# Performance work log

Measured on AMD Instinct MI355X. Metric: run time of the kernel, lower is better.

Reference implementation:

```python
import jax, jax.numpy as jnp
import numpy as np

EPS_RMS = 1e-6
EPS_Q = 1e-5
EPS_NORM = 1e-10


def _rmsnorm(x):
    return x * jax.lax.rsqrt(jnp.mean(x * x, axis=-1, keepdims=True) + EPS_RMS)


def _activation_quant(x):
    # per-token 8-bit absmax quantization (BitNet b1.58)
    scale = 127.0 / jnp.maximum(jnp.max(jnp.abs(x), axis=-1, keepdims=True), EPS_Q)
    return jnp.clip(jnp.round(x * scale), -128.0, 127.0) / scale


def _weight_quant(w):
    # per-tensor ternary quantization with mean-abs scale
    scale = 1.0 / jnp.maximum(jnp.mean(jnp.abs(w)), EPS_Q)
    return jnp.clip(jnp.round(w * scale), -1.0, 1.0) / scale


def _bitlinear(x, w, b):
    xn = _rmsnorm(x)
    xq = xn + jax.lax.stop_gradient(_activation_quant(xn) - xn)  # STE
    wq = w + jax.lax.stop_gradient(_weight_quant(w) - w)         # STE
    return jnp.einsum('bsf,of->bso', xq, wq) + b


def setup_inputs() -> dict:
    key = jax.random.key(0)
    ks = jax.random.split(key, 4)
    B, S, F = 32, 1024, 512
    evidence_features = jax.random.normal(ks[0], (B, S, F), dtype=jnp.float32)
    prior_belief = jax.random.uniform(ks[1], (B, S, F), dtype=jnp.float32)
    W1 = jax.random.normal(ks[2], (F, 2 * F), dtype=jnp.float32) * (1.0 / np.sqrt(2 * F))
    b1 = jnp.zeros((F,), dtype=jnp.float32)
    W2 = jax.random.normal(ks[3], (F, F), dtype=jnp.float32) * (1.0 / np.sqrt(F))
    b2 = jnp.zeros((F,), dtype=jnp.float32)
    return {"evidence_features": evidence_features, "prior_belief": prior_belief,
            "W1": W1, "b1": b1, "W2": W2, "b2": b2}


def reference(evidence_features, prior_belief, W1, b1, W2, b2):
    # belief_update MLP on concat(prior, evidence)
    update_input = jnp.concatenate([prior_belief, evidence_features], axis=-1)  # [B,S,2F]
    h = jax.nn.relu(_bitlinear(update_input, W1, b1))                           # [B,S,F]
    likelihood_factors = jax.nn.sigmoid(_bitlinear(h, W2, b2))                  # [B,S,F]
    posterior_unnorm = prior_belief * likelihood_factors
    normalizer = jnp.maximum(jnp.sum(posterior_unnorm, axis=1, keepdims=True), EPS_NORM)
    return posterior_unnorm / normalizer
```

## Files before the change

kernel.cpp:

```cpp
#include <hip/hip_runtime.h>
#include <math.h>

typedef __attribute__((ext_vector_type(4))) int i32x4;
typedef __attribute__((ext_vector_type(4))) float f32x4;

#define GLOAD_LDS16(g, l)                                          \
  __builtin_amdgcn_global_load_lds(                                \
      (const __attribute__((address_space(1))) void*)(g),          \
      (__attribute__((address_space(3))) void*)(l), 16, 0, 0)

__global__ void kWabs(const float* __restrict__ w1, const float* __restrict__ w2,
                      double* __restrict__ part) {
  const bool second = blockIdx.x >= 256;
  const float* w = second ? w2 : w1;
  const int n = second ? 262144 : 524288;
  int t = (blockIdx.x & 255) * 256 + threadIdx.x;
  double s = 0.0;
  for (int i = t; i < n; i += 65536) s += (double)fabsf(w[i]);
#pragma unroll
  for (int m = 32; m >= 1; m >>= 1) s += __shfl_xor(s, m);
  __shared__ double sd[4];
  int lane = threadIdx.x & 63, wid = threadIdx.x >> 6;
  if (lane == 0) sd[wid] = s;
  __syncthreads();
  if (threadIdx.x == 0) part[blockIdx.x] = (sd[0] + sd[1]) + (sd[2] + sd[3]);
}

__global__ void kWfin(const double* __restrict__ part, float* __restrict__ wsv) {
  const double* p = part + blockIdx.x * 256;
  const double n = (blockIdx.x == 0) ? 524288.0 : 262144.0;
  double s = p[threadIdx.x];
#pragma unroll
  for (int m = 32; m >= 1; m >>= 1) s += __shfl_xor(s, m);
  __shared__ double sd[4];
  int lane = threadIdx.x & 63, wid = threadIdx.x >> 6;
  if (lane == 0) sd[wid] = s;
  __syncthreads();
  if (threadIdx.x == 0) {
    double tot = (sd[0] + sd[1]) + (sd[2] + sd[3]);
    wsv[blockIdx.x] = fmaxf((float)(tot / n), 1e-5f);
  }
}

__global__ void kWq(const float* __restrict__ w1, const float* __restrict__ w2,
                    const float* __restrict__ wsv,
                    char* __restrict__ wq1, char* __restrict__ wq2) {
  const bool second = blockIdx.x >= 2048;
  const float* w = second ? w2 : w1;
  char* wq = second ? wq2 : wq1;
  const float scale = 1.0f / wsv[second ? 1 : 0];
  int i = (second ? blockIdx.x - 2048 : blockIdx.x) * 256 + threadIdx.x;
  float q = fminf(fmaxf(rintf(w[i] * scale), -1.0f), 1.0f);
  wq[i] = (char)(int)q;
}

__global__ __launch_bounds__(512, 1) void kFused1(
    const float* __restrict__ prior, const float* __restrict__ evid,
    const char* __restrict__ Wq, const float* __restrict__ biasG,
    const float* __restrict__ wS,
    char* __restrict__ XqOut, float* __restrict__ rActOut) {
  __shared__ __align__(16) char Ap[65536];
  __shared__ __align__(16) union {
    char B[2][32768];
    struct { float sq[64][8]; float mx[64][8]; } ep;
  } u;
  __shared__ float rowSc[64];
  __shared__ float biasS[512];

  const int tid = threadIdx.x;
  const int lane = tid & 63;
  const int wn = tid >> 6;
  const int lr = lane & 15;
  const int kg = lane >> 4;
  const size_t row0 = (size_t)blockIdx.x * 64;

  biasS[tid] = biasG[tid];

  {
    const float* srcBase = (lane >= 32) ? evid : prior;
    const int lcol = (lane & 31) * 16;
    const int ldsCol = lane * 16;
    const float* sp = srcBase + (row0 + wn * 8) * 512 + lcol;
    f32x4 x0 = ((const f32x4*)sp)[0];
    f32x4 x1 = ((const f32x4*)sp)[1];
    f32x4 x2 = ((const f32x4*)sp)[2];
    f32x4 x3 = ((const f32x4*)sp)[3];
#pragma unroll
    for (int rr = 0; rr < 8; ++rr) {
      f32x4 y0, y1, y2, y3;
      if (rr < 7) {
        const float* np = srcBase + (row0 + wn * 8 + rr + 1) * 512 + lcol;
        y0 = ((const f32x4*)np)[0]; y1 = ((const f32x4*)np)[1];
        y2 = ((const f32x4*)np)[2]; y3 = ((const f32x4*)np)[3];
      }
      float ss = 0.f, mx = 0.f;
      f32x4 xs[4] = {x0, x1, x2, x3};
#pragma unroll
      for (int v = 0; v < 4; ++v)
#pragma unroll
        for (int i = 0; i < 4; ++i) { float f = xs[v][i]; ss += f * f; mx = fmaxf(mx, fabsf(f)); }
#pragma unroll
      for (int m = 32; m >= 1; m >>= 1) { ss += __shfl_xor(ss, m); mx = fmaxf(mx, __shfl_xor(mx, m)); }
      const float inv = 1.0f / sqrtf(ss * (1.0f / 1024.0f) + 1e-6f);
      const float amax = fmaxf(mx * inv, 1e-5f);
      const float s = 127.0f / amax;
      i32x4 q;
#pragma unroll
      for (int v = 0; v < 4; ++v) {
        int p = 0;
#pragma unroll
        for (int i = 0; i < 4; ++i) {
          int qi = (int)fminf(fmaxf(rintf(xs[v][i] * inv * s), -128.0f), 127.0f);
          p |= (qi & 255) << (8 * i);
        }
        q[v] = p;
      }
      const int r = wn * 8 + rr;
      *(i32x4*)&Ap[r * 1024 + (ldsCol ^ ((r & 7) << 4))] = q;
      if (lane == 0) rowSc[r] = amax / 127.0f;
      if (rr < 7) { x0 = y0; x1 = y1; x2 = y2; x3 = y3; }
    }
  }

  i32x4 acc[4][4];
#pragma unroll
  for (int a = 0; a < 4; ++a)
#pragma unroll
    for (int b = 0; b < 4; ++b) acc[a][b] = (i32x4){0, 0, 0, 0};

  const int lrow = lane >> 2;
  const int lkb = (lane & 3) * 16;
  const char* gB[4];
#pragma unroll
  for (int r = 0; r < 4; ++r)
    gB[r] = Wq + ((wn * 4 + r) * 16 + lrow) * (size_t)1024 + lkb;

#define STAGEB(b, k0)                                                \
  do {                                                               \
    _Pragma("unroll")                                                \
    for (int r = 0; r < 4; ++r)                                      \
      GLOAD_LDS16(gB[r] + (k0), &u.B[b][(wn * 4 + r) * 1024]);       \
  } while (0)

  STAGEB(0, 0);
  __syncthreads();

  const int aswz = (lr & 7) << 4;
#pragma unroll 2
  for (int kt = 0; kt < 16; ++kt) {
    const int cur = kt & 1;
    if (kt + 1 < 16) STAGEB(cur ^ 1, (kt + 1) * 64);
    const int acol = (kt * 64 + kg * 16) ^ aswz;
    i32x4 af[4];
#pragma unroll
    for (int fm = 0; fm < 4; ++fm)
      af[fm] = *(const i32x4*)&Ap[(fm * 16 + lr) * 1024 + acol];
#pragma unroll
    for (int fn = 0; fn < 4; ++fn) {
      i32x4 bf = *(const i32x4*)&u.B[cur][(wn * 64 + fn * 16 + lr) * 64 + kg * 16];
#pragma unroll
      for (int fm = 0; fm < 4; ++fm)
        acc[fm][fn] = __builtin_amdgcn_mfma_i32_16x16x64_i8(af[fm], bf, acc[fm][fn], 0, 0, 0);
    }
    __syncthreads();
  }
#undef STAGEB

  const float wsv_ = wS[0];
  f32x4 fa[4][4];
#pragma unroll
  for (int fm = 0; fm < 4; ++fm) {
    float sc[4];
#pragma unroll
    for (int j = 0; j < 4; ++j) sc[j] = rowSc[fm * 16 + kg * 4 + j] * wsv_;
#pragma unroll
    for (int fn = 0; fn < 4; ++fn) {
      const float bb = biasS[wn * 64 + fn * 16 + lr];
#pragma unroll
      for (int j = 0; j < 4; ++j)
        fa[fm][fn][j] = fmaxf((float)acc[fm][fn][j] * sc[j] + bb, 0.0f);
    }
  }
#pragma unroll
  for (int fm = 0; fm < 4; ++fm)
#pragma unroll
    for (int j = 0; j < 4; ++j) {
      float ss = 0.f, mx = 0.f;
#pragma unroll
      for (int fn = 0; fn < 4; ++fn) { float h = fa[fm][fn][j]; ss += h * h; mx = fmaxf(mx, h); }
#pragma unroll
      for (int m = 8; m >= 1; m >>= 1) { ss += __shfl_xor(ss, m); mx = fmaxf(mx, __shfl_xor(mx, m)); }
      if (lr == 0) {
        int rl = fm * 16 + kg * 4 + j;
        u.ep.sq[rl][wn] = ss;
        u.ep.mx[rl][wn] = mx;
      }
    }
  __syncthreads();
#pragma unroll
  for (int fm = 0; fm < 4; ++fm)
#pragma unroll
    for (int j = 0; j < 4; ++j) {
      const int rl = fm * 16 + kg * 4 + j;
      float sst = 0.f, mxt = 0.f;
#pragma unroll
      for (int w = 0; w < 8; ++w) {
        sst += u.ep.sq[rl][w];
        mxt = fmaxf(mxt, u.ep.mx[rl][w]);
      }
      float inv = 1.0f / sqrtf(sst * (1.0f / 512.0f) + 1e-6f);
      float amax = fmaxf(mxt * inv, 1e-5f);
      float s = 127.0f / amax;
      if (lr == 0 && wn == 0) rActOut[row0 + rl] = amax / 127.0f;
#pragma unroll
      for (int fn = 0; fn < 4; ++fn) {
        float xn = fa[fm][fn][j] * inv;
        int qi = (int)fminf(fmaxf(rintf(xn * s), -128.0f), 127.0f);
        XqOut[(row0 + rl) * 512 + wn * 64 + fn * 16 + lr] = (char)qi;
      }
    }
}

__global__ __launch_bounds__(512, 4) void kGemm2(
    const char* __restrict__ Xq, const char* __restrict__ Wq,
    const float* __restrict__ biasG, const float* __restrict__ rAct,
    const float* __restrict__ wS, const float* __restrict__ prior,
    float* __restrict__ outUn, float* __restrict__ partG) {
  constexpr int KDIM = 512;
  struct Stage { char A[4096]; char B[32768]; };
  __shared__ __align__(16) Stage st[2];
  __shared__ float rowR[64];
  __shared__ float biasS[512];
  __shared__ float normPart[512];

  const int tid = threadIdx.x;
  const int lane = tid & 63;
  const int wn = tid >> 6;
  const int lr = lane & 15;
  const int kg = lane >> 4;
  const size_t row0 = (size_t)blockIdx.x * 64;

  if (tid < 64) rowR[tid] = rAct[row0 + tid];
  biasS[tid] = biasG[tid];

  i32x4 acc[4][4];
#pragma unroll
  for (int a = 0; a < 4; ++a)
#pragma unroll
    for (int b = 0; b < 4; ++b) acc[a][b] = (i32x4){0, 0, 0, 0};

  const int lrow = lane >> 2;
  const int lkb = (lane & 3) * 16;
  const char* gA = Xq + (row0 + (wn & 3) * 16 + lrow) * (size_t)KDIM + lkb;
  const char* gB[4];
#pragma unroll
  for (int r = 0; r < 4; ++r)
    gB[r] = Wq + ((wn * 4 + r) * 16 + lrow) * (size_t)KDIM + lkb;

#define STAGE(b, k0)                                                 \
  do {                                                               \
    if (wn < 4) GLOAD_LDS16(gA + (k0), &st[b].A[(wn & 3) * 1024]);   \
    _Pragma("unroll")                                                \
    for (int r = 0; r < 4; ++r)                                      \
      GLOAD_LDS16(gB[r] + (k0), &st[b].B[(wn * 4 + r) * 1024]);      \
  } while (0)

  constexpr int NT = KDIM / 64;
  STAGE(0, 0);
  __syncthreads();

#pragma unroll 2
  for (int kt = 0; kt < NT; ++kt) {
    const int cur = kt & 1;
    if (kt + 1 < NT) STAGE(cur ^ 1, (kt + 1) * 64);
    i32x4 af[4];
#pragma unroll
    for (int fm = 0; fm < 4; ++fm)
      af[fm] = *(const i32x4*)&st[cur].A[(fm * 16 + lr) * 64 + kg * 16];
#pragma unroll
    for (int fn = 0; fn < 4; ++fn) {
      i32x4 bf = *(const i32x4*)&st[cur].B[(wn * 64 + fn * 16 + lr) * 64 + kg * 16];
#pragma unroll
      for (int fm = 0; fm < 4; ++fm)
        acc[fm][fn] = __builtin_amdgcn_mfma_i32_16x16x64_i8(af[fm], bf, acc[fm][fn], 0, 0, 0);
    }
    __syncthreads();
  }
#undef STAGE

  const float wsv_ = wS[0];
  float colsum[4] = {0.f, 0.f, 0.f, 0.f};
#pragma unroll
  for (int fm = 0; fm < 4; ++fm) {
    float sc[4];
#pragma unroll
    for (int j = 0; j < 4; ++j) sc[j] = rowR[fm * 16 + kg * 4 + j] * wsv_;
#pragma unroll
    for (int fn = 0; fn < 4; ++fn) {
      const int col = wn * 64 + fn * 16 + lr;
      const float bb = biasS[col];
#pragma unroll
      for (int j = 0; j < 4; ++j) {
        const size_t rg = row0 + fm * 16 + kg * 4 + j;
        float v = (float)acc[fm][fn][j] * sc[j] + bb;
        float like = 1.0f / (1.0f + expf(-v));
        float un = prior[rg * 512 + col] * like;
        outUn[rg * 512 + col] = un;
        colsum[fn] += un;
      }
    }
  }
#pragma unroll
  for (int fn = 0; fn < 4; ++fn) {
    colsum[fn] += __shfl_xor(colsum[fn], 16);
    colsum[fn] += __shfl_xor(colsum[fn], 32);
  }
  if (lane < 16) {
#pragma unroll
    for (int fn = 0; fn < 4; ++fn) normPart[wn * 64 + fn * 16 + lane] = colsum[fn];
  }
  __syncthreads();
  partG[(size_t)blockIdx.x * 512 + tid] = normPart[tid];
}

__global__ void kNorm1(const float* __restrict__ partG, float* __restrict__ normA) {
  const int b = blockIdx.x, f = threadIdx.x;
  float s = 0.f;
#pragma unroll
  for (int i = 0; i < 16; ++i) s += partG[(size_t)(b * 16 + i) * 512 + f];
  normA[b * 512 + f] = fmaxf(s, 1e-10f);
}

__global__ void kNorm2(float* __restrict__ out, const float* __restrict__ normA) {
  const size_t i4 = (size_t)blockIdx.x * blockDim.x + threadIdx.x;
  f32x4 v = ((const f32x4*)out)[i4];
  const int f4 = (int)(i4 & 127);
  const int b = (int)(i4 >> 17);
  f32x4 n = ((const f32x4*)normA)[b * 128 + f4];
  v[0] /= n[0]; v[1] /= n[1]; v[2] /= n[2]; v[3] /= n[3];
  ((f32x4*)out)[i4] = v;
}

extern "C" void kernel_launch(void* const* d_in, const int* in_sizes, int n_in,
                              void* d_out, int out_size, void* d_ws, size_t ws_size,
                              hipStream_t stream) {
  const float* evid  = (const float*)d_in[0];
  const float* prior = (const float*)d_in[1];
  const float* W1    = (const float*)d_in[2];
  const float* b1    = (const float*)d_in[3];
  const float* W2    = (const float*)d_in[4];
  const float* b2    = (const float*)d_in[5];
  float* out = (float*)d_out;

  char* ws = (char*)d_ws;
  char*   X2q   = ws;
  char*   W1q   = ws + 16777216;
  char*   W2q   = ws + 17301504;
  float*  r2    = (float*)(ws + 17563648);
  double* part  = (double*)(ws + 17694720);
  float*  wsv   = (float*)(ws + 17698816);
  float*  partG = (float*)(ws + 17699072);
  float*  normA = (float*)(ws + 18747648);

  kWabs<<<512, 256, 0, stream>>>(W1, W2, part);
  kWfin<<<2, 256, 0, stream>>>(part, wsv);
  kWq<<<3072, 256, 0, stream>>>(W1, W2, wsv, W1q, W2q);
  kFused1<<<512, 512, 0, stream>>>(prior, evid, W1q, b1, wsv + 0, X2q, r2);
  kGemm2<<<512, 512, 0, stream>>>(X2q, W2q, b2, r2, wsv + 1, prior, out, partG);
  kNorm1<<<32, 512, 0, stream>>>(partG, normA);
  kNorm2<<<16384, 256, 0, stream>>>(out, normA);
}
```

Before: 136.8 us.

## Load weight fragments directly to registers and drop LDS double buffering

```diff
diff --git a/kernel.cpp b/kernel.cpp
--- a/kernel.cpp
+++ b/kernel.cpp
@@ -54,14 +54,13 @@
   wq[i] = (char)(int)q;
 }
 
-__global__ __launch_bounds__(512, 1) void kFused1(
+__global__ __launch_bounds__(512, 4) void kFused1(
     const float* __restrict__ prior, const float* __restrict__ evid,
     const char* __restrict__ Wq, const float* __restrict__ biasG,
     const float* __restrict__ wS,
     char* __restrict__ XqOut, float* __restrict__ rActOut) {
-  __shared__ __align__(16) char Ap[65536];
   __shared__ __align__(16) union {
-    char B[2][32768];
+    char Ap[65536];
     struct { float sq[64][8]; float mx[64][8]; } ep;
   } u;
   __shared__ float rowSc[64];
@@ -116,7 +115,7 @@
         q[v] = p;
       }
       const int r = wn * 8 + rr;
-      *(i32x4*)&Ap[r * 1024 + (ldsCol ^ ((r & 7) << 4))] = q;
+      *(i32x4*)&u.Ap[r * 1024 + (ldsCol ^ ((r & 7) << 4))] = q;
       if (lane == 0) rowSc[r] = amax / 127.0f;
       if (rr < 7) { x0 = y0; x1 = y1; x2 = y2; x3 = y3; }
     }
@@ -128,43 +127,38 @@
 #pragma unroll
     for (int b = 0; b < 4; ++b) acc[a][b] = (i32x4){0, 0, 0, 0};
 
-  const int lrow = lane >> 2;
-  const int lkb = (lane & 3) * 16;
-  const char* gB[4];
-#pragma unroll
-  for (int r = 0; r < 4; ++r)
-    gB[r] = Wq + ((wn * 4 + r) * 16 + lrow) * (size_t)1024 + lkb;
-
-#define STAGEB(b, k0)                                                \
-  do {                                                               \
-    _Pragma("unroll")                                                \
-    for (int r = 0; r < 4; ++r)                                      \
-      GLOAD_LDS16(gB[r] + (k0), &u.B[b][(wn * 4 + r) * 1024]);       \
-  } while (0)
-
-  STAGEB(0, 0);
+  const char* gBl = Wq + (size_t)(wn * 64 + lr) * 1024 + kg * 16;
+  i32x4 bf[4];
+#pragma unroll
+  for (int fn = 0; fn < 4; ++fn)
+    bf[fn] = *(const i32x4*)(gBl + fn * 16384);
+
   __syncthreads();
 
   const int aswz = (lr & 7) << 4;
 #pragma unroll 2
   for (int kt = 0; kt < 16; ++kt) {
-    const int cur = kt & 1;
-    if (kt + 1 < 16) STAGEB(cur ^ 1, (kt + 1) * 64);
+    i32x4 bn[4];
+    if (kt < 15) {
+#pragma unroll
+      for (int fn = 0; fn < 4; ++fn)
+        bn[fn] = *(const i32x4*)(gBl + (kt + 1) * 64 + fn * 16384);
+    }
     const int acol = (kt * 64 + kg * 16) ^ aswz;
     i32x4 af[4];
 #pragma unroll
     for (int fm = 0; fm < 4; ++fm)
-      af[fm] = *(const i32x4*)&Ap[(fm * 16 + lr) * 1024 + acol];
-#pragma unroll
-    for (int fn = 0; fn < 4; ++fn) {
-      i32x4 bf = *(const i32x4*)&u.B[cur][(wn * 64 + fn * 16 + lr) * 64 + kg * 16];
+      af[fm] = *(const i32x4*)&u.Ap[(fm * 16 + lr) * 1024 + acol];
+#pragma unroll
+    for (int fn = 0; fn < 4; ++fn)
 #pragma unroll
       for (int fm = 0; fm < 4; ++fm)
-        acc[fm][fn] = __builtin_amdgcn_mfma_i32_16x16x64_i8(af[fm], bf, acc[fm][fn], 0, 0, 0);
-    }
-    __syncthreads();
-  }
-#undef STAGEB
+        acc[fm][fn] = __builtin_amdgcn_mfma_i32_16x16x64_i8(af[fm], bf[fn], acc[fm][fn], 0, 0, 0);
+#pragma unroll
+    for (int fn = 0; fn < 4; ++fn) bf[fn] = bn[fn];
+  }
+
+  __syncthreads();
 
   const float wsv_ = wS[0];
   f32x4 fa[4][4];
@@ -226,9 +220,7 @@
     const float* __restrict__ biasG, const float* __restrict__ rAct,
     const float* __restrict__ wS, const float* __restrict__ prior,
     float* __restrict__ outUn, float* __restrict__ partG) {
-  constexpr int KDIM = 512;
-  struct Stage { char A[4096]; char B[32768]; };
-  __shared__ __align__(16) Stage st[2];
+  __shared__ __align__(16) char A[32768];
   __shared__ float rowR[64];
   __shared__ float biasS[512];
   __shared__ float normPart[512];
@@ -243,50 +235,49 @@
   if (tid < 64) rowR[tid] = rAct[row0 + tid];
   biasS[tid] = biasG[tid];
 
+#pragma unroll
+  for (int i = 0; i < 4; ++i) {
+    const int r = i * 16 + wn * 2 + (lane >> 5);
+    const int cs = ((lane & 31) * 16) ^ ((r & 7) << 4);
+    GLOAD_LDS16(Xq + (row0 + r) * 512 + cs, &A[i * 8192 + wn * 1024]);
+  }
+
+  const char* gBl = Wq + (size_t)(wn * 64 + lr) * 512 + kg * 16;
+  i32x4 bf[4];
+#pragma unroll
+  for (int fn = 0; fn < 4; ++fn)
+    bf[fn] = *(const i32x4*)(gBl + fn * 8192);
+
   i32x4 acc[4][4];
 #pragma unroll
   for (int a = 0; a < 4; ++a)
 #pragma unroll
     for (int b = 0; b < 4; ++b) acc[a][b] = (i32x4){0, 0, 0, 0};
 
-  const int lrow = lane >> 2;
-  const int lkb = (lane & 3) * 16;
-  const char* gA = Xq + (row0 + (wn & 3) * 16 + lrow) * (size_t)KDIM + lkb;
-  const char* gB[4];
-#pragma unroll
-  for (int r = 0; r < 4; ++r)
-    gB[r] = Wq + ((wn * 4 + r) * 16 + lrow) * (size_t)KDIM + lkb;
-
-#define STAGE(b, k0)                                                 \
-  do {                                                               \
-    if (wn < 4) GLOAD_LDS16(gA + (k0), &st[b].A[(wn & 3) * 1024]);   \
-    _Pragma("unroll")                                                \
-    for (int r = 0; r < 4; ++r)                                      \
-      GLOAD_LDS16(gB[r] + (k0), &st[b].B[(wn * 4 + r) * 1024]);      \
-  } while (0)
-
-  constexpr int NT = KDIM / 64;
-  STAGE(0, 0);
-  __syncthreads();
-
+  __syncthreads();
+
+  const int aswz = (lr & 7) << 4;
 #pragma unroll 2
-  for (int kt = 0; kt < NT; ++kt) {
-    const int cur = kt & 1;
-    if (kt + 1 < NT) STAGE(cur ^ 1, (kt + 1) * 64);
+  for (int kt = 0; kt < 8; ++kt) {
+    i32x4 bn[4];
+    if (kt < 7) {
+#pragma unroll
+      for (int fn = 0; fn < 4; ++fn)
+        bn[fn] = *(const i32x4*)(gBl + (kt + 1) * 64 + fn * 8192);
+    }
+    const int acol = (kt * 64 + kg * 16) ^ aswz;
     i32x4 af[4];
 #pragma unroll
     for (int fm = 0; fm < 4; ++fm)
-      af[fm] = *(const i32x4*)&st[cur].A[(fm * 16 + lr) * 64 + kg * 16];
-#pragma unroll
-    for (int fn = 0; fn < 4; ++fn) {
-      i32x4 bf = *(const i32x4*)&st[cur].B[(wn * 64 + fn * 16 + lr) * 64 + kg * 16];
+      af[fm] = *(const i32x4*)&A[(fm * 16 + lr) * 512 + acol];
+#pragma unroll
+    for (int fn = 0; fn < 4; ++fn)
 #pragma unroll
       for (int fm = 0; fm < 4; ++fm)
-        acc[fm][fn] = __builtin_amdgcn_mfma_i32_16x16x64_i8(af[fm], bf, acc[fm][fn], 0, 0, 0);
-    }
-    __syncthreads();
-  }
-#undef STAGE
+        acc[fm][fn] = __builtin_amdgcn_mfma_i32_16x16x64_i8(af[fm], bf[fn], acc[fm][fn], 0, 0, 0);
+#pragma unroll
+    for (int fn = 0; fn < 4; ++fn) bf[fn] = bn[fn];
+  }
 
   const float wsv_ = wS[0];
   float colsum[4] = {0.f, 0.f, 0.f, 0.f};
```

After: 135.4 us (median of 2 runs). No clear change (-1.0%).
